# Kernel optimization log

Hardware: AMD Instinct MI355X
Metric: run time of the kernel (lower is better)

## Reference

```python
import jax, jax.numpy as jnp
import numpy as np

RETRIEVAL_SHARPNESS = 50.0
TWO_PI = 2.0 * np.pi


def setup_inputs() -> dict:
    key = jax.random.key(0)
    k1, k2, k3, k4 = jax.random.split(key, 4)
    W, S = 4096, 4096
    return {
        "hologram_re": jax.random.normal(k1, (W, S), dtype=jnp.float32),
        "hologram_im": jax.random.normal(k2, (W, S), dtype=jnp.float32),
        "cue_re": jax.random.normal(k3, (W, S), dtype=jnp.float32),
        "cue_im": jax.random.normal(k4, (W, S), dtype=jnp.float32),
        "n_keys": 1024,
    }


def _make_keys(n_keys, W):
    # write(): key_idx -> exp(1j * arange(W) * (idx+1)*2pi/W), stacked [N, W]
    freqs = (jnp.arange(n_keys, dtype=jnp.float32) + 1.0) * (TWO_PI / W)  # [N]
    phase = freqs[:, None] * jnp.arange(W, dtype=jnp.float32)[None, :]    # [N, W]
    return jnp.exp(1j * phase)  # complex64 [N, W]


def reference(hologram_re, hologram_im, cue_re, cue_im, n_keys):
    W, S = hologram_re.shape
    holo = hologram_re + 1j * hologram_im  # [W, S] complex64
    cue = cue_re + 1j * cue_im             # [W, S] complex64
    keys = _make_keys(n_keys, W)            # [N, W]

    # noisy_mix = (hologram * cue.conj()).sum(dim=1) -> [W]
    noisy_mix = jnp.sum(holo * jnp.conj(cue), axis=1)
    # correlations = |dot(noisy_mix, k)| per key (torch.dot: no conjugation)
    correlations = jnp.abs(keys @ noisy_mix)  # [N]
    attention = jax.nn.softmax(correlations * RETRIEVAL_SHARPNESS)  # [N]
    # clean_key = sum_k attention[k] * keys[k] -> [W]
    clean_key = attention.astype(keys.dtype) @ keys
    out = holo * clean_key[:, None]  # [W, S] complex64
    return jnp.stack([out.real, out.imag])  # [2, W, S] float32
```

## Files before the change

### kernel.cpp

```cpp
#include <hip/hip_runtime.h>
#include <math.h>

#define W 4096
#define S 4096
#define NK_MAX 1024

typedef float v4f __attribute__((ext_vector_type(4)));


__global__ void prep_kernel(float2* __restrict__ table) {
    int k = blockIdx.x * blockDim.x + threadIdx.x;
    if (k >= W) return;
    double theta = (double)k * (6.283185307179586 / (double)W);
    table[k] = make_float2((float)cos(theta), (float)sin(theta));
}

__global__ void nm_kernel(const float* __restrict__ hr, const float* __restrict__ hi,
                          const float* __restrict__ cr, const float* __restrict__ ci,
                          float2* __restrict__ nm) {
    int w = blockIdx.x;
    int t = threadIdx.x;
    size_t base = (size_t)w * 1024;
    const v4f* hr4 = (const v4f*)hr;
    const v4f* hi4 = (const v4f*)hi;
    const v4f* cr4 = (const v4f*)cr;
    const v4f* ci4 = (const v4f*)ci;

    v4f a[4], b[4], c[4], d[4];
#pragma unroll
    for (int k = 0; k < 4; k++) {
        size_t i = base + t + k * 256;
        a[k] = hr4[i];
        b[k] = hi4[i];
        c[k] = __builtin_nontemporal_load(&cr4[i]);
        d[k] = __builtin_nontemporal_load(&ci4[i]);
    }
    v4f vr = {0.f, 0.f, 0.f, 0.f}, vi = {0.f, 0.f, 0.f, 0.f};
#pragma unroll
    for (int k = 0; k < 4; k++) {
        vr += a[k] * c[k] + b[k] * d[k];
        vi += b[k] * c[k] - a[k] * d[k];
    }
    float sr = vr.x + vr.y + vr.z + vr.w;
    float si = vi.x + vi.y + vi.z + vi.w;

    for (int off = 32; off; off >>= 1) {
        sr += __shfl_down(sr, off);
        si += __shfl_down(si, off);
    }
    __shared__ float s0[4], s1[4];
    int lane = t & 63, wid = t >> 6;
    if (lane == 0) { s0[wid] = sr; s1[wid] = si; }
    __syncthreads();
    if (t == 0) {
        nm[w] = make_float2(s0[0] + s0[1] + s0[2] + s0[3],
                            s1[0] + s1[1] + s1[2] + s1[3]);
    }
}

__global__ void corr_kernel(const float2* __restrict__ nm, const float2* __restrict__ table,
                            float* __restrict__ corr, const int* __restrict__ nkp) {
    int n = blockIdx.x;
    if (n >= *nkp) return;
    int f = n + 1;
    float sr = 0.f, si = 0.f;
    for (int w = threadIdx.x; w < W; w += 256) {
        int idx = (w * f) & (W - 1);
        float2 t = table[idx];
        float2 v = nm[w];
        sr += t.x * v.x - t.y * v.y;
        si += t.x * v.y + t.y * v.x;
    }
    for (int off = 32; off; off >>= 1) {
        sr += __shfl_down(sr, off);
        si += __shfl_down(si, off);
    }
    __shared__ float s0[4], s1[4];
    int lane = threadIdx.x & 63, wid = threadIdx.x >> 6;
    if (lane == 0) { s0[wid] = sr; s1[wid] = si; }
    __syncthreads();
    if (threadIdx.x == 0) {
        float r = s0[0] + s0[1] + s0[2] + s0[3];
        float m = s1[0] + s1[1] + s1[2] + s1[3];
        corr[n] = sqrtf(r * r + m * m);
    }
}

__global__ void ck_kernel(const float* __restrict__ corr, const float2* __restrict__ table,
                          float2* __restrict__ ck, const int* __restrict__ nkp) {
    __shared__ float2 stab[W];
    __shared__ float satt[NK_MAX];
    __shared__ float red[8];
    int t = threadIdx.x;
    int nk = *nkp;
    int lane = t & 63, wid = t >> 6;

    for (int i = t; i < W; i += 256) stab[i] = table[i];

    float v[4];
    float vmax = -INFINITY;
    for (int j = 0; j < 4; j++) {
        int i = t + j * 256;
        v[j] = (i < nk) ? corr[i] * 50.0f : -INFINITY;
        vmax = fmaxf(vmax, v[j]);
    }
    for (int off = 32; off; off >>= 1) vmax = fmaxf(vmax, __shfl_down(vmax, off));
    if (lane == 0) red[wid] = vmax;
    __syncthreads();
    float M = fmaxf(fmaxf(red[0], red[1]), fmaxf(red[2], red[3]));
    __syncthreads();

    float esum = 0.f;
    for (int j = 0; j < 4; j++) {
        int i = t + j * 256;
        float e = (i < nk) ? expf(v[j] - M) : 0.f;
        if (i < NK_MAX) satt[i] = e;
        esum += e;
    }
    for (int off = 32; off; off >>= 1) esum += __shfl_down(esum, off);
    if (lane == 0) red[4 + wid] = esum;
    __syncthreads();
    float SUM = red[4] + red[5] + red[6] + red[7];

    int wl = t >> 2, sub = t & 3;
    int w = blockIdx.x * 64 + wl;
    int n0 = sub * 256;
    float crr = 0.f, cii = 0.f;
    int idx = (int)(((long long)w * (n0 + 1)) & (W - 1));
    int nend = min(n0 + 256, nk);
    for (int n = n0; n < nend; n++) {
        float2 tt = stab[idx];
        float a = satt[n];
        crr += a * tt.x;
        cii += a * tt.y;
        idx = (idx + w) & (W - 1);
    }
    crr += __shfl_xor(crr, 1); cii += __shfl_xor(cii, 1);
    crr += __shfl_xor(crr, 2); cii += __shfl_xor(cii, 2);
    if (sub == 0 && w < W) ck[w] = make_float2(crr / SUM, cii / SUM);
}

__global__ void out_kernel(const float* __restrict__ hr, const float* __restrict__ hi,
                           const float2* __restrict__ ck, float* __restrict__ out) {
    int w = blockIdx.x;
    int t = threadIdx.x;
    size_t base = (size_t)w * 1024;
    const size_t total4 = (size_t)W * S / 4;
    float2 c = ck[w];

    v4f a[4], b[4];
#pragma unroll
    for (int k = 0; k < 4; k++) {
        size_t i = base + t + k * 256;
        a[k] = ((const v4f*)hr)[i];
        b[k] = ((const v4f*)hi)[i];
    }
#pragma unroll
    for (int k = 0; k < 4; k++) {
        size_t i = base + t + k * 256;
        v4f re = a[k] * c.x - b[k] * c.y;
        v4f im = a[k] * c.y + b[k] * c.x;
        __builtin_nontemporal_store(re, &((v4f*)out)[i]);
        __builtin_nontemporal_store(im, &((v4f*)out)[i + total4]);
    }
}

extern "C" void kernel_launch(void* const* d_in, const int* in_sizes, int n_in,
                              void* d_out, int out_size, void* d_ws, size_t ws_size,
                              hipStream_t stream) {
    const float* hr = (const float*)d_in[0];
    const float* hi = (const float*)d_in[1];
    const float* cr = (const float*)d_in[2];
    const float* ci = (const float*)d_in[3];
    const int* nk = (const int*)d_in[4];

    float* ws = (float*)d_ws;
    float2* table = (float2*)ws;
    float2* nm    = (float2*)(ws + 8192);
    float* corr   = ws + 16384;
    float2* ck    = (float2*)(ws + 17408);
    float* out = (float*)d_out;

    prep_kernel<<<W / 256, 256, 0, stream>>>(table);
    nm_kernel<<<W, 256, 0, stream>>>(hr, hi, cr, ci, nm);
    corr_kernel<<<NK_MAX, 256, 0, stream>>>(nm, table, corr, nk);
    ck_kernel<<<W / 64, 256, 0, stream>>>(corr, table, ck, nk);
    out_kernel<<<W, 256, 0, stream>>>(hr, hi, ck, out);
}
```

Before: 357.5 us.

## Fuse table prep into nm kernel and softmax/clean-key into output kernel

Moves the twiddle-table generation into the noisy-mix kernel, one entry per block. Folds the softmax and clean-key computation into the output kernel so each row block computes its own clean-key value. This cuts five launches down to three and removes the ck round trip through memory. In exchange every one of the 4096 output blocks recomputes the full softmax over corr and gathers table entries. That adds redundant work and barriers before the streaming stores.

```diff
diff --git a/kernel.cpp b/kernel.cpp
--- a/kernel.cpp
+++ b/kernel.cpp
@@ -8,16 +8,9 @@
 typedef float v4f __attribute__((ext_vector_type(4)));
 
 
-__global__ void prep_kernel(float2* __restrict__ table) {
-    int k = blockIdx.x * blockDim.x + threadIdx.x;
-    if (k >= W) return;
-    double theta = (double)k * (6.283185307179586 / (double)W);
-    table[k] = make_float2((float)cos(theta), (float)sin(theta));
-}
-
 __global__ void nm_kernel(const float* __restrict__ hr, const float* __restrict__ hi,
                           const float* __restrict__ cr, const float* __restrict__ ci,
-                          float2* __restrict__ nm) {
+                          float2* __restrict__ nm, float2* __restrict__ table) {
     int w = blockIdx.x;
     int t = threadIdx.x;
     size_t base = (size_t)w * 1024;
@@ -35,6 +28,12 @@
         c[k] = __builtin_nontemporal_load(&cr4[i]);
         d[k] = __builtin_nontemporal_load(&ci4[i]);
     }
+
+    if (t == 0) {
+        double theta = (double)w * (6.283185307179586 / (double)W);
+        table[w] = make_float2((float)cos(theta), (float)sin(theta));
+    }
+
     v4f vr = {0.f, 0.f, 0.f, 0.f}, vi = {0.f, 0.f, 0.f, 0.f};
 #pragma unroll
     for (int k = 0; k < 4; k++) {
@@ -86,19 +85,29 @@
     }
 }
 
-__global__ void ck_kernel(const float* __restrict__ corr, const float2* __restrict__ table,
-                          float2* __restrict__ ck, const int* __restrict__ nkp) {
-    __shared__ float2 stab[W];
-    __shared__ float satt[NK_MAX];
+__global__ void out_kernel(const float* __restrict__ hr, const float* __restrict__ hi,
+                           const float* __restrict__ corr, const float2* __restrict__ table,
+                           const int* __restrict__ nkp, float* __restrict__ out) {
+    int w = blockIdx.x;
+    int t = threadIdx.x;
+    size_t base = (size_t)w * 1024;
+    const size_t total4 = (size_t)W * S / 4;
+    int lane = t & 63, wid = t >> 6;
     __shared__ float red[8];
-    int t = threadIdx.x;
+
+    v4f a[4], b[4];
+#pragma unroll
+    for (int k = 0; k < 4; k++) {
+        size_t i = base + t + k * 256;
+        a[k] = ((const v4f*)hr)[i];
+        b[k] = ((const v4f*)hi)[i];
+    }
+
     int nk = *nkp;
-    int lane = t & 63, wid = t >> 6;
-
-    for (int i = t; i < W; i += 256) stab[i] = table[i];
 
     float v[4];
     float vmax = -INFINITY;
+#pragma unroll
     for (int j = 0; j < 4; j++) {
         int i = t + j * 256;
         v[j] = (i < nk) ? corr[i] * 50.0f : -INFINITY;
@@ -108,58 +117,46 @@
     if (lane == 0) red[wid] = vmax;
     __syncthreads();
     float M = fmaxf(fmaxf(red[0], red[1]), fmaxf(red[2], red[3]));
-    __syncthreads();
 
+    float e[4];
     float esum = 0.f;
+#pragma unroll
     for (int j = 0; j < 4; j++) {
         int i = t + j * 256;
-        float e = (i < nk) ? expf(v[j] - M) : 0.f;
-        if (i < NK_MAX) satt[i] = e;
-        esum += e;
+        e[j] = (i < nk) ? expf(v[j] - M) : 0.f;
+        esum += e[j];
     }
     for (int off = 32; off; off >>= 1) esum += __shfl_down(esum, off);
     if (lane == 0) red[4 + wid] = esum;
     __syncthreads();
     float SUM = red[4] + red[5] + red[6] + red[7];
+    __syncthreads();
 
-    int wl = t >> 2, sub = t & 3;
-    int w = blockIdx.x * 64 + wl;
-    int n0 = sub * 256;
     float crr = 0.f, cii = 0.f;
-    int idx = (int)(((long long)w * (n0 + 1)) & (W - 1));
-    int nend = min(n0 + 256, nk);
-    for (int n = n0; n < nend; n++) {
-        float2 tt = stab[idx];
-        float a = satt[n];
-        crr += a * tt.x;
-        cii += a * tt.y;
-        idx = (idx + w) & (W - 1);
+#pragma unroll
+    for (int j = 0; j < 4; j++) {
+        int i = t + j * 256;
+        if (i < nk) {
+            int idx = (w * (i + 1)) & (W - 1);
+            float2 tt = table[idx];
+            crr += e[j] * tt.x;
+            cii += e[j] * tt.y;
+        }
     }
-    crr += __shfl_xor(crr, 1); cii += __shfl_xor(cii, 1);
-    crr += __shfl_xor(crr, 2); cii += __shfl_xor(cii, 2);
-    if (sub == 0 && w < W) ck[w] = make_float2(crr / SUM, cii / SUM);
-}
+    for (int off = 32; off; off >>= 1) {
+        crr += __shfl_down(crr, off);
+        cii += __shfl_down(cii, off);
+    }
+    if (lane == 0) { red[wid] = crr; red[4 + wid] = cii; }
+    __syncthreads();
+    float ckr = (red[0] + red[1] + red[2] + red[3]) / SUM;
+    float cki = (red[4] + red[5] + red[6] + red[7]) / SUM;
 
-__global__ void out_kernel(const float* __restrict__ hr, const float* __restrict__ hi,
-                           const float2* __restrict__ ck, float* __restrict__ out) {
-    int w = blockIdx.x;
-    int t = threadIdx.x;
-    size_t base = (size_t)w * 1024;
-    const size_t total4 = (size_t)W * S / 4;
-    float2 c = ck[w];
-
-    v4f a[4], b[4];
 #pragma unroll
     for (int k = 0; k < 4; k++) {
         size_t i = base + t + k * 256;
-        a[k] = ((const v4f*)hr)[i];
-        b[k] = ((const v4f*)hi)[i];
-    }
-#pragma unroll
-    for (int k = 0; k < 4; k++) {
-        size_t i = base + t + k * 256;
-        v4f re = a[k] * c.x - b[k] * c.y;
-        v4f im = a[k] * c.y + b[k] * c.x;
+        v4f re = a[k] * ckr - b[k] * cki;
+        v4f im = a[k] * cki + b[k] * ckr;
         __builtin_nontemporal_store(re, &((v4f*)out)[i]);
         __builtin_nontemporal_store(im, &((v4f*)out)[i + total4]);
     }
@@ -178,12 +175,9 @@
     float2* table = (float2*)ws;
     float2* nm    = (float2*)(ws + 8192);
     float* corr   = ws + 16384;
-    float2* ck    = (float2*)(ws + 17408);
     float* out = (float*)d_out;
 
-    prep_kernel<<<W / 256, 256, 0, stream>>>(table);
-    nm_kernel<<<W, 256, 0, stream>>>(hr, hi, cr, ci, nm);
+    nm_kernel<<<W, 256, 0, stream>>>(hr, hi, cr, ci, nm, table);
     corr_kernel<<<NK_MAX, 256, 0, stream>>>(nm, table, corr, nk);
-    ck_kernel<<<W / 64, 256, 0, stream>>>(corr, table, ck, nk);
-    out_kernel<<<W, 256, 0, stream>>>(hr, hi, ck, out);
+    out_kernel<<<W, 256, 0, stream>>>(hr, hi, corr, table, nk, out);
 }
```

Result: faster. 337.0 us (-5.7%).
